# Optimization experiments

Measured on AMD Instinct MI355X. Metric: run time of the kernel, lower is better.

## Reference

```python
import jax, jax.numpy as jnp
import numpy as np

B, CIN, COUT, N, R = 8, 64, 64, 32768, 32
R3 = R * R * R
BN_EPS = 1e-4


def leaky(x):
    return jnp.where(x >= 0, x, 0.1 * x)


def bn(x, gamma, beta, axes, bshape):
    # training-mode batchnorm (batch statistics)
    m = x.mean(axes, keepdims=True)
    v = x.var(axes, keepdims=True)
    return (x - m) * jax.lax.rsqrt(v + BN_EPS) * gamma.reshape(bshape) + beta.reshape(bshape)


def conv3d(x, w, b):
    y = jax.lax.conv_general_dilated(
        x, w, window_strides=(1, 1, 1), padding=[(1, 1)] * 3,
        dimension_numbers=('NCDHW', 'OIDHW', 'NCDHW'))
    return y + b[None, :, None, None, None]


def setup_inputs() -> dict:
    key = jax.random.key(0)
    ks = jax.random.split(key, 6)
    f32 = jnp.float32
    return {
        'features': jax.random.normal(ks[0], (B, CIN, N), f32),
        'coords': jax.random.normal(ks[1], (B, 3, N), f32),
        'w1': jax.random.normal(ks[2], (COUT, CIN, 3, 3, 3), f32) * 0.05,
        'b1': jnp.zeros((COUT,), f32),
        'g1': jnp.ones((COUT,), f32),
        'beta1': jnp.zeros((COUT,), f32),
        'w2': jax.random.normal(ks[3], (COUT, COUT, 3, 3, 3), f32) * 0.05,
        'b2': jnp.zeros((COUT,), f32),
        'g2': jnp.ones((COUT,), f32),
        'beta2': jnp.zeros((COUT,), f32),
        'wp': jax.random.normal(ks[4], (COUT, CIN), f32) * 0.05,
        'bp': jnp.zeros((COUT,), f32),
        'gp': jnp.ones((COUT,), f32),
        'betap': jnp.zeros((COUT,), f32),
    }


def _norm_coords(coords):
    # Voxelization coordinate normalization (normalize=True, eps=0)
    nc = coords - coords.mean(axis=2, keepdims=True)                      # [B,3,N]
    mag = jnp.linalg.norm(nc, axis=1, keepdims=True)                      # [B,1,N]
    nc = nc / (mag.max(axis=2, keepdims=True) * 2.0) + 0.5
    return jnp.clip(nc * R, 0.0, R - 1)                                   # [B,3,N] in [0, R-1]


def _voxelize(features, norm):
    vox = jnp.round(norm).astype(jnp.int32)                               # [B,3,N]
    flat = (vox[:, 0] * R + vox[:, 1]) * R + vox[:, 2]                    # [B,N]

    def scat(f, idx):  # f: [C,N], idx: [N]
        s = jax.ops.segment_sum(f.T, idx, num_segments=R3)                # [R3,C]
        c = jax.ops.segment_sum(jnp.ones(idx.shape, f.dtype), idx, num_segments=R3)
        return (s / jnp.maximum(c, 1.0)[:, None]).T                       # [C,R3]

    return jax.vmap(scat)(features, flat)                                 # [B,C,R3]


def _devoxelize(grid_flat, norm):
    # trilinear gather: grid_flat [B,C,R3], norm [B,3,N] -> [B,C,N]
    lo = jnp.floor(norm).astype(jnp.int32)
    frac = norm - lo
    hi = jnp.clip(lo + 1, 0, R - 1)
    gather = jax.vmap(lambda gf, i: gf[:, i])  # per-batch fancy gather
    out = jnp.zeros((grid_flat.shape[0], grid_flat.shape[1], norm.shape[2]), grid_flat.dtype)
    for dx in (0, 1):
        for dy in (0, 1):
            for dz in (0, 1):
                xi = hi[:, 0] if dx else lo[:, 0]
                yi = hi[:, 1] if dy else lo[:, 1]
                zi = hi[:, 2] if dz else lo[:, 2]
                w = ((frac[:, 0] if dx else 1.0 - frac[:, 0]) *
                     (frac[:, 1] if dy else 1.0 - frac[:, 1]) *
                     (frac[:, 2] if dz else 1.0 - frac[:, 2]))            # [B,N]
                idx = (xi * R + yi) * R + zi                               # [B,N]
                out = out + gather(grid_flat, idx) * w[:, None, :]
    return out


def reference(features, coords, w1, b1, g1, beta1, w2, b2, g2, beta2, wp, bp, gp, betap):
    norm = _norm_coords(coords)
    grid = _voxelize(features, norm).reshape(B, CIN, R, R, R)
    x = leaky(bn(conv3d(grid, w1, b1), g1, beta1, (0, 2, 3, 4), (1, COUT, 1, 1, 1)))
    x = leaky(bn(conv3d(x, w2, b2), g2, beta2, (0, 2, 3, 4), (1, COUT, 1, 1, 1)))
    voxel_feats = _devoxelize(x.reshape(B, COUT, R3), norm)               # [B,COUT,N]
    # point branch: SharedMLP = 1x1 Conv1d + BN1d + ReLU
    p = jnp.einsum('oc,bcn->bon', wp, features) + bp[None, :, None]
    p = jax.nn.relu(bn(p, gp, betap, (0, 2), (1, COUT, 1)))
    return voxel_feats + p
```

## Files before the change

kernel.cpp:

```cpp
#include <hip/hip_runtime.h>

typedef __attribute__((ext_vector_type(8))) short short8;
typedef __attribute__((ext_vector_type(8))) unsigned short ushort8;
typedef __attribute__((ext_vector_type(4))) unsigned short ushort4v;
typedef __attribute__((ext_vector_type(4))) float f32x4;
typedef unsigned int uint;
typedef unsigned short ushort;

#define BB 8
#define CC 64
#define NPT 32768
#define RR 32
#define R3 32768
#define RP 34
#define RP2 1156
#define RP3 39304
#define BN_EPS 1e-4f

__device__ __forceinline__ ushort f2bf(float x) {
    uint u = __float_as_uint(x);
    u = (u + 0x7FFFu + ((u >> 16) & 1u)) >> 16;
    return (ushort)u;
}
__device__ __forceinline__ float bf2f(ushort u) {
    return __uint_as_float(((uint)u) << 16);
}
__device__ __forceinline__ void gload_lds16(const void* g, void* l) {
    __builtin_amdgcn_global_load_lds(
        (const __attribute__((address_space(1))) unsigned int*)g,
        (__attribute__((address_space(3))) unsigned int*)l, 16, 0, 0);
}

__global__ void k_mean(const float* __restrict__ coords, float* __restrict__ mean) {
    __shared__ float sbuf[256];
    int bd = blockIdx.x;
    const float* c = coords + (size_t)bd * NPT;
    float s = 0.f;
    for (int i = threadIdx.x; i < NPT; i += 256) s += c[i];
    sbuf[threadIdx.x] = s; __syncthreads();
    for (int off = 128; off > 0; off >>= 1) {
        if (threadIdx.x < off) sbuf[threadIdx.x] += sbuf[threadIdx.x + off];
        __syncthreads();
    }
    if (threadIdx.x == 0) mean[bd] = sbuf[0] / (float)NPT;
}

__global__ void k_maxmag(const float* __restrict__ coords, const float* __restrict__ mean,
                         float* __restrict__ maxmag) {
    __shared__ float sbuf[256];
    int b = blockIdx.x;
    float m0 = mean[b*3], m1 = mean[b*3+1], m2 = mean[b*3+2];
    const float* c = coords + (size_t)b * 3 * NPT;
    float mx = 0.f;
    for (int i = threadIdx.x; i < NPT; i += 256) {
        float x = c[i] - m0, y = c[NPT + i] - m1, z = c[2*NPT + i] - m2;
        mx = fmaxf(mx, x*x + y*y + z*z);
    }
    sbuf[threadIdx.x] = mx; __syncthreads();
    for (int off = 128; off > 0; off >>= 1) {
        if (threadIdx.x < off) sbuf[threadIdx.x] = fmaxf(sbuf[threadIdx.x], sbuf[threadIdx.x + off]);
        __syncthreads();
    }
    if (threadIdx.x == 0) maxmag[b] = sqrtf(sbuf[0]);
}

__global__ void k_norm(const float* __restrict__ coords, const float* __restrict__ mean,
                       const float* __restrict__ maxmag,
                       float* __restrict__ norm, int* __restrict__ nxt, int* __restrict__ head) {
    int b = blockIdx.y;
    int n = blockIdx.x * 256 + threadIdx.x;
    float denom = maxmag[b] * 2.0f;
    int vi[3];
    #pragma unroll
    for (int d = 0; d < 3; d++) {
        float v = (coords[((size_t)b*3 + d)*NPT + n] - mean[b*3 + d]) / denom + 0.5f;
        v *= (float)RR;
        v = fminf(fmaxf(v, 0.0f), (float)(RR - 1));
        norm[((size_t)b*3 + d)*NPT + n] = v;
        vi[d] = (int)rintf(v);
    }
    int pf = ((vi[0]+1)*RP + (vi[1]+1))*RP + (vi[2]+1);
    nxt[b*NPT + n] = atomicExch(&head[b*RP3 + pf], n);
}

__global__ __launch_bounds__(256) void k_transpose(const float* __restrict__ feat,
                                                   ushort* __restrict__ featT) {
    __shared__ float t[64][65];
    int b = blockIdx.y;
    int n0 = blockIdx.x * 64;
    for (int i = threadIdx.x; i < 4096; i += 256) {
        int ci = i >> 6, nl = i & 63;
        t[ci][nl] = feat[((size_t)(b*CC + ci))*NPT + n0 + nl];
    }
    __syncthreads();
    for (int i = threadIdx.x; i < 4096; i += 256) {
        int nl = i >> 6, ci = i & 63;
        featT[((size_t)b*NPT + n0 + nl)*64 + ci] = f2bf(t[ci][nl]);
    }
}

__global__ __launch_bounds__(256) void k_gather(const ushort* __restrict__ featT,
                                                const int* __restrict__ head,
                                                const int* __restrict__ nxt,
                                                ushort* __restrict__ gbf) {
    int b = blockIdx.y;
    int v = blockIdx.x * 4 + (threadIdx.x >> 6);
    int lane = threadIdx.x & 63;
    float a = 0.f;
    int c = 0;
    int p = head[b*RP3 + v];
    while (p >= 0) {
        a += bf2f(featT[((size_t)b*NPT + p)*64 + lane]);
        c++;
        p = nxt[b*NPT + p];
    }
    float r = (c > 0) ? a / (float)c : 0.f;
    gbf[((size_t)((b*2 + (lane >> 5))*RP3) + v)*32 + (lane & 31)] = f2bf(r);
}

__global__ void k_wt(const float* __restrict__ w, ushort* __restrict__ wT) {
    int s = blockIdx.x * 256 + threadIdx.x;
    int ci = s & 31;
    int co = (s >> 5) & 63;
    int t  = (s >> 11) % 27;
    int ch = s / 55296;
    wT[s] = f2bf(w[(size_t)co*1728 + (size_t)(ch*32 + ci)*27 + t]);
}

__global__ void k_bnpack(const ushort* __restrict__ raw,
                         const float* __restrict__ gs, const float* __restrict__ gq,
                         const float* __restrict__ gamma, const float* __restrict__ beta,
                         ushort* __restrict__ gbf) {
    __shared__ float s_sc[64], s_sh[64];
    if (threadIdx.x < 64) {
        int c = threadIdx.x;
        const float cntf = 262144.0f;
        float m = gs[c] / cntf;
        float vv = gq[c] / cntf - m*m;
        float scv = gamma[c] * rsqrtf(fmaxf(vv, 0.0f) + BN_EPS);
        s_sc[c] = scv;
        s_sh[c] = beta[c] - m*scv;
    }
    __syncthreads();
    int s = blockIdx.x * 256 + threadIdx.x;
    int j = s & 3;
    int tmp = s >> 2;
    int v = tmp % RP3;
    int t2 = tmp / RP3;
    int ch = t2 & 1, b = t2 >> 1;
    int gz = v / RP2; int r = v - gz*RP2;
    int gy = r / RP;  int gx = r - gy*RP;
    ushort8 o;
    if (gz >= 1 && gz <= 32 && gy >= 1 && gy <= 32 && gx >= 1 && gx <= 32) {
        int uvox = ((gz-1)*RR + (gy-1))*RR + (gx-1);
        int cb = ch*32 + j*8;
        ushort8 rv = *(const ushort8*)(raw + ((size_t)b*R3 + uvox)*64 + cb);
        #pragma unroll
        for (int e = 0; e < 8; e++) {
            float x = bf2f(rv[e])*s_sc[cb + e] + s_sh[cb + e];
            x = x >= 0.f ? x : 0.1f*x;
            o[e] = f2bf(x);
        }
    } else {
        #pragma unroll
        for (int e = 0; e < 8; e++) o[e] = 0;
    }
    *(ushort8*)(gbf + ((size_t)((b*2 + ch)*RP3) + v)*32 + j*8) = o;
}

__global__ __launch_bounds__(512) void k_conv_mfma(
    const ushort* __restrict__ gbf,
    const ushort* __restrict__ wT,
    ushort* __restrict__ rawbf,
    float* __restrict__ gs, float* __restrict__ gq)
{
    __shared__ uint4 lds4[2 * 3888];
    const int d0r = blockIdx.x;
    const int d0 = (d0r & 7) * 4 + (d0r >> 3);
    const int quad = blockIdx.y, b = blockIdx.z;
    const int y0 = (quad >> 1) * 16, x0 = (quad & 1) * 16;
    const int tid = threadIdx.x;
    const int lane = tid & 63;
    const int wid = tid >> 6;
    const int mgroup = wid & 1, ngroup = wid >> 1;
    const int l15 = lane & 15, kgrp = lane >> 4;

    f32x4 acc[2][4];
    #pragma unroll
    for (int mf = 0; mf < 2; mf++)
        #pragma unroll
        for (int f = 0; f < 4; f++) acc[mf][f] = (f32x4)(0.0f);

    const int coA = mgroup*32 + l15;
    const int coB = coA + 16;

    {
        const char* gbase = (const char*)gbf + (size_t)(b*2 + 0) * ((size_t)RP3 * 64);
        for (int c = tid; c < 3888; c += 512) {
            int row = c >> 2, j = c & 3;
            int z = row / 324; int rem = row - z*324;
            int y = rem / 18;  int xl = rem - y*18;
            int srcj = j ^ ((xl >> 1) & 3);
            const char* src = gbase +
                (size_t)((d0 + z)*RP2 + (y0 + y)*RP + (x0 + xl)) * 64 + srcj*16;
            gload_lds16(src, (char*)lds4 + c*16);
        }
    }
    __syncthreads();
    {
        const char* gbase = (const char*)gbf + (size_t)(b*2 + 1) * ((size_t)RP3 * 64);
        for (int c = tid; c < 3888; c += 512) {
            int row = c >> 2, j = c & 3;
            int z = row / 324; int rem = row - z*324;
            int y = rem / 18;  int xl = rem - y*18;
            int srcj = j ^ ((xl >> 1) & 3);
            const char* src = gbase +
                (size_t)((d0 + z)*RP2 + (y0 + y)*RP + (x0 + xl)) * 64 + srcj*16;
            gload_lds16(src, (char*)lds4 + 62208 + c*16);
        }
    }

    #pragma unroll
    for (int ch = 0; ch < 2; ch++) {
        if (ch == 1) __syncthreads();
        const char* lbase = (const char*)lds4 + ch * 62208;
        const ushort* wbase = wT + (size_t)ch * 27 * 2048 + kgrp*8;
        short8 wq[3][2];
        #pragma unroll
        for (int pre = 0; pre < 3; pre++) {
            wq[pre][0] = *(const short8*)(wbase + (size_t)pre*2048 + coA*32);
            wq[pre][1] = *(const short8*)(wbase + (size_t)pre*2048 + coB*32);
        }
        __builtin_amdgcn_s_setprio(1);
        #pragma unroll
        for (int t = 0; t < 27; t++) {
            const int t0 = t / 9, t1 = (t / 3) % 3, t2 = t % 3;
            const int slot = t % 3;
            int x = l15 + t2;
            int inrow = (kgrp ^ ((x >> 1) & 3)) << 4;
            #pragma unroll
            for (int f = 0; f < 4; f++) {
                int y = ngroup*4 + f + t1;
                int vox = (t0*18 + y)*18 + x;
                short8 bfr = *(const short8*)(lbase + vox*64 + inrow);
                acc[0][f] = __builtin_amdgcn_mfma_f32_16x16x32_bf16(wq[slot][0], bfr, acc[0][f], 0, 0, 0);
                acc[1][f] = __builtin_amdgcn_mfma_f32_16x16x32_bf16(wq[slot][1], bfr, acc[1][f], 0, 0, 0);
            }
            if (t + 3 < 27) {
                wq[slot][0] = *(const short8*)(wbase + (size_t)(t+3)*2048 + coA*32);
                wq[slot][1] = *(const short8*)(wbase + (size_t)(t+3)*2048 + coB*32);
            }
        }
        __builtin_amdgcn_s_setprio(0);
    }
    int d2 = x0 + l15;
    #pragma unroll
    for (int f = 0; f < 4; f++) {
        int d1 = y0 + ngroup*4 + f;
        int vox = (d0*RR + d1)*RR + d2;
        ushort* dst = rawbf + ((size_t)b*R3 + vox)*64 + mgroup*32 + kgrp*4;
        ushort4v o0, o1;
        #pragma unroll
        for (int e = 0; e < 4; e++) { o0[e] = f2bf(acc[0][f][e]); o1[e] = f2bf(acc[1][f][e]); }
        *(ushort4v*)dst = o0;
        *(ushort4v*)(dst + 16) = o1;
    }
    __syncthreads();
    float* bins = (float*)lds4;
    if (tid < 128) bins[tid] = 0.f;
    __syncthreads();
    float sv[2][4], qv[2][4];
    #pragma unroll
    for (int mf = 0; mf < 2; mf++)
        #pragma unroll
        for (int e = 0; e < 4; e++) {
            float s = 0.f, q = 0.f;
            #pragma unroll
            for (int f = 0; f < 4; f++) {
                float v = acc[mf][f][e];
                s += v; q += v*v;
            }
            #pragma unroll
            for (int m = 1; m < 16; m <<= 1) {
                s += __shfl_xor(s, m);
                q += __shfl_xor(q, m);
            }
            sv[mf][e] = s; qv[mf][e] = q;
        }
    if (l15 == 0) {
        #pragma unroll
        for (int mf = 0; mf < 2; mf++)
            #pragma unroll
            for (int e = 0; e < 4; e++) {
                int co = mgroup*32 + mf*16 + kgrp*4 + e;
                atomicAdd(&bins[co], sv[mf][e]);
                atomicAdd(&bins[64 + co], qv[mf][e]);
            }
    }
    __syncthreads();
    if (tid < 64) { atomicAdd(&gs[tid], bins[tid]); atomicAdd(&gq[tid], bins[64 + tid]); }
}

__global__ __launch_bounds__(256) void k_point_stats_P(const ushort* __restrict__ featT,
                                                       const float* __restrict__ wp,
                                                       ushort* __restrict__ P,
                                                       float* __restrict__ gs,
                                                       float* __restrict__ gq) {
    __shared__ float ls[64], lq[64];
    int b = blockIdx.y;
    int n = blockIdx.x * 256 + threadIdx.x;
    if (threadIdx.x < 64) { ls[threadIdx.x] = 0.f; lq[threadIdx.x] = 0.f; }
    __syncthreads();
    f32x4 fr[16];
    const ushort8* fp = (const ushort8*)(featT + ((size_t)b*NPT + n)*64);
    #pragma unroll
    for (int r = 0; r < 8; r++) {
        ushort8 u = fp[r];
        #pragma unroll
        for (int e = 0; e < 8; e++)
            fr[(r*8 + e) >> 2][(r*8 + e) & 3] = bf2f(u[e]);
    }
    int lane = threadIdx.x & 63;
    #pragma unroll
    for (int co = 0; co < 64; co++) {
        float p = 0.f;
        #pragma unroll
        for (int r = 0; r < 16; r++) {
            f32x4 w4 = *(const f32x4*)(wp + co*64 + r*4);
            p = fmaf(w4[0], fr[r][0], p); p = fmaf(w4[1], fr[r][1], p);
            p = fmaf(w4[2], fr[r][2], p); p = fmaf(w4[3], fr[r][3], p);
        }
        P[((size_t)(b*64 + co))*NPT + n] = f2bf(p);
        float s = p, q = p*p;
        #pragma unroll
        for (int m = 1; m < 64; m <<= 1) {
            s += __shfl_xor(s, m);
            q += __shfl_xor(q, m);
        }
        if (lane == 0) { atomicAdd(&ls[co], s); atomicAdd(&lq[co], q); }
    }
    __syncthreads();
    if (threadIdx.x < 64) {
        atomicAdd(&gs[threadIdx.x], ls[threadIdx.x]);
        atomicAdd(&gq[threadIdx.x], lq[threadIdx.x]);
    }
}

__global__ __launch_bounds__(256) void k_final4(
    const ushort* __restrict__ x2raw,
    const float* __restrict__ norm,
    const ushort* __restrict__ P,
    const float* __restrict__ gs2, const float* __restrict__ gq2,
    const float* __restrict__ g2, const float* __restrict__ be2,
    const float* __restrict__ gsp, const float* __restrict__ gqp,
    const float* __restrict__ gp, const float* __restrict__ bep,
    float* __restrict__ out)
{
    __shared__ float s_sc[64], s_sh[64], s_scp[64], s_shp[64];
    int b = blockIdx.y;
    int tid = threadIdx.x;
    const float cntf = 262144.0f;
    if (tid < 64) {
        int c = tid;
        float m = gs2[c] / cntf;
        float vv = gq2[c] / cntf - m*m;
        float scv = g2[c] * rsqrtf(fmaxf(vv, 0.0f) + BN_EPS);
        s_sc[c] = scv; s_sh[c] = be2[c] - m*scv;
    } else if (tid < 128) {
        int c = tid - 64;
        float m = gsp[c] / cntf;
        float vv = gqp[c] / cntf - m*m;
        float scv = gp[c] * rsqrtf(fmaxf(vv, 0.0f) + BN_EPS);
        s_scp[c] = scv; s_shp[c] = bep[c] - m*scv;
    }
    __syncthreads();
    int pt = blockIdx.x * 64 + (tid & 63);
    int q = tid >> 6;
    float v0 = norm[((size_t)b*3 + 0)*NPT + pt];
    float v1 = norm[((size_t)b*3 + 1)*NPT + pt];
    float v2 = norm[((size_t)b*3 + 2)*NPT + pt];
    int l0 = (int)floorf(v0), l1 = (int)floorf(v1), l2 = (int)floorf(v2);
    float f0 = v0 - (float)l0, f1 = v1 - (float)l1, f2 = v2 - (float)l2;
    int h0 = min(l0 + 1, RR - 1), h1 = min(l1 + 1, RR - 1), h2 = min(l2 + 1, RR - 1);

    f32x4 scv[4], shv[4];
    #pragma unroll
    for (int r = 0; r < 4; r++) {
        scv[r] = *(const f32x4*)&s_sc[q*16 + r*4];
        shv[r] = *(const f32x4*)&s_sh[q*16 + r*4];
    }

    f32x4 a4[4];
    #pragma unroll
    for (int r = 0; r < 4; r++) a4[r] = (f32x4)(0.0f);
    #pragma unroll
    for (int c = 0; c < 8; c++) {
        int xi = (c & 4) ? h0 : l0; float wx = (c & 4) ? f0 : 1.f - f0;
        int yi = (c & 2) ? h1 : l1; float wy = (c & 2) ? f1 : 1.f - f1;
        int zi = (c & 1) ? h2 : l2; float wz = (c & 1) ? f2 : 1.f - f2;
        float w = wx * wy * wz;
        const ushort* g = x2raw +
            ((size_t)b*R3 + (size_t)((xi*RR + yi)*RR + zi))*64 + q*16;
        ushort8 rv0 = *(const ushort8*)g;
        ushort8 rv1 = *(const ushort8*)(g + 8);
        #pragma unroll
        for (int r = 0; r < 2; r++) {
            #pragma unroll
            for (int e = 0; e < 4; e++) {
                float x = bf2f(rv0[r*4 + e])*scv[r][e] + shv[r][e];
                x = x >= 0.f ? x : 0.1f*x;
                a4[r][e] = fmaf(w, x, a4[r][e]);
                float x2 = bf2f(rv1[r*4 + e])*scv[2 + r][e] + shv[2 + r][e];
                x2 = x2 >= 0.f ? x2 : 0.1f*x2;
                a4[2 + r][e] = fmaf(w, x2, a4[2 + r][e]);
            }
        }
    }
    #pragma unroll
    for (int r = 0; r < 4; r++) {
        #pragma unroll
        for (int e = 0; e < 4; e++) {
            int co = q*16 + r*4 + e;
            float p = bf2f(P[((size_t)(b*64 + co))*NPT + pt]);
            p = p * s_scp[co] + s_shp[co];
            p = fmaxf(p, 0.f);
            out[((size_t)(b*64 + co))*NPT + pt] = a4[r][e] + p;
        }
    }
}

extern "C" void kernel_launch(void* const* d_in, const int* in_sizes, int n_in,
                              void* d_out, int out_size, void* d_ws, size_t ws_size,
                              hipStream_t stream) {
    const float* feat   = (const float*)d_in[0];
    const float* coords = (const float*)d_in[1];
    const float* w1  = (const float*)d_in[2];
    const float* g1  = (const float*)d_in[4];
    const float* be1 = (const float*)d_in[5];
    const float* w2  = (const float*)d_in[6];
    const float* g2  = (const float*)d_in[8];
    const float* be2 = (const float*)d_in[9];
    const float* wp  = (const float*)d_in[10];
    const float* gp  = (const float*)d_in[12];
    const float* bep = (const float*)d_in[13];
    float* out = (float*)d_out;
    float* ws  = (float*)d_ws;

    float* mean   = ws;
    float* maxmag = ws + 24;
    float* stats  = ws + 32;
    float* norm   = ws + 1024;
    int*   nxt    = (int*)(ws + 787456);
    int*   head   = (int*)(ws + 1049600);
    ushort* rawbf = (ushort*)(ws + 1364032);
    ushort* wT1   = (ushort*)(ws + 21487680);
    ushort* wT2   = (ushort*)(ws + 21542976);
    ushort* gbf   = (ushort*)(ws + 21598272);
    ushort* P     = (ushort*)(ws + 21598272);
    ushort* featT = (ushort*)(ws + 31660096);

    hipMemsetAsync(stats, 0, 384 * sizeof(float), stream);
    hipMemsetAsync(head, 0xFF, 314432ull * sizeof(int), stream);

    k_wt<<<432, 256, 0, stream>>>(w1, wT1);
    k_wt<<<432, 256, 0, stream>>>(w2, wT2);

    k_mean  <<<24, 256, 0, stream>>>(coords, mean);
    k_maxmag<<<8, 256, 0, stream>>>(coords, mean, maxmag);
    k_norm  <<<dim3(128, 8), 256, 0, stream>>>(coords, mean, maxmag, norm, nxt, head);
    k_transpose<<<dim3(512, 8), 256, 0, stream>>>(feat, featT);
    k_gather<<<dim3(9826, 8), 256, 0, stream>>>(featT, head, nxt, gbf);

    k_conv_mfma<<<dim3(32, 4, 8), 512, 0, stream>>>(gbf, wT1, rawbf, stats + 0, stats + 64);
    k_bnpack<<<9826, 256, 0, stream>>>(rawbf, stats + 0, stats + 64, g1, be1, gbf);

    k_conv_mfma<<<dim3(32, 4, 8), 512, 0, stream>>>(gbf, wT2, rawbf, stats + 128, stats + 192);

    k_point_stats_P<<<dim3(128, 8), 256, 0, stream>>>(featT, wp, P, stats + 256, stats + 320);

    k_final4<<<dim3(512, 8), 256, 0, stream>>>(rawbf, norm, P,
                                               stats + 128, stats + 192, g2, be2,
                                               stats + 256, stats + 320, gp, bep,
                                               out);
}
```

Before: 494.8 us.

## Fuse coord prep kernels, merge weight transposes, store point-MLP output point-major

Merges the mean, max-magnitude and normalize/link-list kernels into one per-batch 1024-thread kernel, and folds the two weight-transpose launches into one. The point MLP now writes its bf16 output in place over featT, in point-major layout with vector stores, and the final kernel reads it with two 16-byte loads instead of 16 strided scalar loads. This cuts launch count and makes the P write and read coalesced. The cost is that normalization now runs on only 8 blocks, which serializes a pass over the coordinates that was previously spread across 1024 blocks.

Result: slower. 557.2 us (+12.6%).

```diff
diff --git a/kernel.cpp b/kernel.cpp
--- a/kernel.cpp
+++ b/kernel.cpp
@@ -31,56 +31,53 @@
         (__attribute__((address_space(3))) unsigned int*)l, 16, 0, 0);
 }
 
-__global__ void k_mean(const float* __restrict__ coords, float* __restrict__ mean) {
-    __shared__ float sbuf[256];
-    int bd = blockIdx.x;
-    const float* c = coords + (size_t)bd * NPT;
-    float s = 0.f;
-    for (int i = threadIdx.x; i < NPT; i += 256) s += c[i];
-    sbuf[threadIdx.x] = s; __syncthreads();
-    for (int off = 128; off > 0; off >>= 1) {
-        if (threadIdx.x < off) sbuf[threadIdx.x] += sbuf[threadIdx.x + off];
+__global__ __launch_bounds__(1024) void k_prep(const float* __restrict__ coords,
+                                               float* __restrict__ norm,
+                                               int* __restrict__ nxt, int* __restrict__ head) {
+    __shared__ float sb[1024];
+    __shared__ float sm[4];
+    int b = blockIdx.x;
+    int tid = threadIdx.x;
+    const float* cb = coords + (size_t)b * 3 * NPT;
+    #pragma unroll
+    for (int d = 0; d < 3; d++) {
+        float s = 0.f;
+        for (int i = tid; i < NPT; i += 1024) s += cb[(size_t)d*NPT + i];
+        sb[tid] = s; __syncthreads();
+        for (int off = 512; off > 0; off >>= 1) {
+            if (tid < off) sb[tid] += sb[tid + off];
+            __syncthreads();
+        }
+        if (tid == 0) sm[d] = sb[0] / (float)NPT;
         __syncthreads();
     }
-    if (threadIdx.x == 0) mean[bd] = sbuf[0] / (float)NPT;
-}
-
-__global__ void k_maxmag(const float* __restrict__ coords, const float* __restrict__ mean,
-                         float* __restrict__ maxmag) {
-    __shared__ float sbuf[256];
-    int b = blockIdx.x;
-    float m0 = mean[b*3], m1 = mean[b*3+1], m2 = mean[b*3+2];
-    const float* c = coords + (size_t)b * 3 * NPT;
+    float m0 = sm[0], m1 = sm[1], m2 = sm[2];
     float mx = 0.f;
-    for (int i = threadIdx.x; i < NPT; i += 256) {
-        float x = c[i] - m0, y = c[NPT + i] - m1, z = c[2*NPT + i] - m2;
+    for (int i = tid; i < NPT; i += 1024) {
+        float x = cb[i] - m0, y = cb[NPT + i] - m1, z = cb[2*NPT + i] - m2;
         mx = fmaxf(mx, x*x + y*y + z*z);
     }
-    sbuf[threadIdx.x] = mx; __syncthreads();
-    for (int off = 128; off > 0; off >>= 1) {
-        if (threadIdx.x < off) sbuf[threadIdx.x] = fmaxf(sbuf[threadIdx.x], sbuf[threadIdx.x + off]);
+    sb[tid] = mx; __syncthreads();
+    for (int off = 512; off > 0; off >>= 1) {
+        if (tid < off) sb[tid] = fmaxf(sb[tid], sb[tid + off]);
         __syncthreads();
     }
-    if (threadIdx.x == 0) maxmag[b] = sqrtf(sbuf[0]);
-}
-
-__global__ void k_norm(const float* __restrict__ coords, const float* __restrict__ mean,
-                       const float* __restrict__ maxmag,
-                       float* __restrict__ norm, int* __restrict__ nxt, int* __restrict__ head) {
-    int b = blockIdx.y;
-    int n = blockIdx.x * 256 + threadIdx.x;
-    float denom = maxmag[b] * 2.0f;
-    int vi[3];
-    #pragma unroll
-    for (int d = 0; d < 3; d++) {
-        float v = (coords[((size_t)b*3 + d)*NPT + n] - mean[b*3 + d]) / denom + 0.5f;
-        v *= (float)RR;
-        v = fminf(fmaxf(v, 0.0f), (float)(RR - 1));
-        norm[((size_t)b*3 + d)*NPT + n] = v;
-        vi[d] = (int)rintf(v);
-    }
-    int pf = ((vi[0]+1)*RP + (vi[1]+1))*RP + (vi[2]+1);
-    nxt[b*NPT + n] = atomicExch(&head[b*RP3 + pf], n);
+    if (tid == 0) sm[3] = sqrtf(sb[0]) * 2.0f;
+    __syncthreads();
+    float denom = sm[3];
+    for (int n = tid; n < NPT; n += 1024) {
+        float v0 = (cb[n] - m0) / denom + 0.5f;
+        float v1 = (cb[NPT + n] - m1) / denom + 0.5f;
+        float v2 = (cb[2*NPT + n] - m2) / denom + 0.5f;
+        v0 = fminf(fmaxf(v0 * (float)RR, 0.f), (float)(RR - 1));
+        v1 = fminf(fmaxf(v1 * (float)RR, 0.f), (float)(RR - 1));
+        v2 = fminf(fmaxf(v2 * (float)RR, 0.f), (float)(RR - 1));
+        norm[((size_t)b*3 + 0)*NPT + n] = v0;
+        norm[((size_t)b*3 + 1)*NPT + n] = v1;
+        norm[((size_t)b*3 + 2)*NPT + n] = v2;
+        int pf = (((int)rintf(v0)+1)*RP + ((int)rintf(v1)+1))*RP + ((int)rintf(v2)+1);
+        nxt[b*NPT + n] = atomicExch(&head[b*RP3 + pf], n);
+    }
 }
 
 __global__ __launch_bounds__(256) void k_transpose(const float* __restrict__ feat,
@@ -118,13 +115,17 @@
     gbf[((size_t)((b*2 + (lane >> 5))*RP3) + v)*32 + (lane & 31)] = f2bf(r);
 }
 
-__global__ void k_wt(const float* __restrict__ w, ushort* __restrict__ wT) {
+__global__ void k_wt2(const float* __restrict__ w1, const float* __restrict__ w2,
+                      ushort* __restrict__ wT1, ushort* __restrict__ wT2) {
     int s = blockIdx.x * 256 + threadIdx.x;
-    int ci = s & 31;
-    int co = (s >> 5) & 63;
-    int t  = (s >> 11) % 27;
-    int ch = s / 55296;
-    wT[s] = f2bf(w[(size_t)co*1728 + (size_t)(ch*32 + ci)*27 + t]);
+    const float* w = (s < 110592) ? w1 : w2;
+    ushort* wT = (s < 110592) ? wT1 : wT2;
+    int si = (s < 110592) ? s : s - 110592;
+    int ci = si & 31;
+    int co = (si >> 5) & 63;
+    int t  = (si >> 11) % 27;
+    int ch = si / 55296;
+    wT[si] = f2bf(w[(size_t)co*1728 + (size_t)(ch*32 + ci)*27 + t]);
 }
 
 __global__ void k_bnpack(const ushort* __restrict__ raw,
@@ -301,9 +302,8 @@
     if (tid < 64) { atomicAdd(&gs[tid], bins[tid]); atomicAdd(&gq[tid], bins[64 + tid]); }
 }
 
-__global__ __launch_bounds__(256) void k_point_stats_P(const ushort* __restrict__ featT,
+__global__ __launch_bounds__(256) void k_point_stats_P(ushort* __restrict__ featT,
                                                        const float* __restrict__ wp,
-                                                       ushort* __restrict__ P,
                                                        float* __restrict__ gs,
                                                        float* __restrict__ gq) {
     __shared__ float ls[64], lq[64];
@@ -311,26 +311,29 @@
     int n = blockIdx.x * 256 + threadIdx.x;
     if (threadIdx.x < 64) { ls[threadIdx.x] = 0.f; lq[threadIdx.x] = 0.f; }
     __syncthreads();
-    f32x4 fr[16];
-    const ushort8* fp = (const ushort8*)(featT + ((size_t)b*NPT + n)*64);
-    #pragma unroll
-    for (int r = 0; r < 8; r++) {
-        ushort8 u = fp[r];
-        #pragma unroll
-        for (int e = 0; e < 8; e++)
-            fr[(r*8 + e) >> 2][(r*8 + e) & 3] = bf2f(u[e]);
+    ushort* rowp = featT + ((size_t)b*NPT + n)*64;
+    float fr[64];
+    {
+        const ushort8* fp = (const ushort8*)rowp;
+        #pragma unroll
+        for (int r = 0; r < 8; r++) {
+            ushort8 u = fp[r];
+            #pragma unroll
+            for (int e = 0; e < 8; e++) fr[r*8 + e] = bf2f(u[e]);
+        }
     }
     int lane = threadIdx.x & 63;
+    float ps[64];
     #pragma unroll
     for (int co = 0; co < 64; co++) {
         float p = 0.f;
         #pragma unroll
         for (int r = 0; r < 16; r++) {
             f32x4 w4 = *(const f32x4*)(wp + co*64 + r*4);
-            p = fmaf(w4[0], fr[r][0], p); p = fmaf(w4[1], fr[r][1], p);
-            p = fmaf(w4[2], fr[r][2], p); p = fmaf(w4[3], fr[r][3], p);
-        }
-        P[((size_t)(b*64 + co))*NPT + n] = f2bf(p);
+            p = fmaf(w4[0], fr[r*4+0], p); p = fmaf(w4[1], fr[r*4+1], p);
+            p = fmaf(w4[2], fr[r*4+2], p); p = fmaf(w4[3], fr[r*4+3], p);
+        }
+        ps[co] = p;
         float s = p, q = p*p;
         #pragma unroll
         for (int m = 1; m < 64; m <<= 1) {
@@ -338,6 +341,13 @@
             q += __shfl_xor(q, m);
         }
         if (lane == 0) { atomicAdd(&ls[co], s); atomicAdd(&lq[co], q); }
+    }
+    #pragma unroll
+    for (int g = 0; g < 8; g++) {
+        ushort8 o;
+        #pragma unroll
+        for (int e = 0; e < 8; e++) o[e] = f2bf(ps[g*8 + e]);
+        *(ushort8*)(rowp + g*8) = o;
     }
     __syncthreads();
     if (threadIdx.x < 64) {
@@ -416,12 +426,16 @@
             }
         }
     }
+    const ushort* pr = P + ((size_t)b*NPT + pt)*64 + q*16;
+    ushort8 pv0 = *(const ushort8*)pr;
+    ushort8 pv1 = *(const ushort8*)(pr + 8);
     #pragma unroll
     for (int r = 0; r < 4; r++) {
         #pragma unroll
         for (int e = 0; e < 4; e++) {
-            int co = q*16 + r*4 + e;
-            float p = bf2f(P[((size_t)(b*64 + co))*NPT + pt]);
+            int idx = r*4 + e;
+            int co = q*16 + idx;
+            float p = bf2f(idx < 8 ? pv0[idx] : pv1[idx - 8]);
             p = p * s_scp[co] + s_shp[co];
             p = fmaxf(p, 0.f);
             out[((size_t)(b*64 + co))*NPT + pt] = a4[r][e] + p;
@@ -446,8 +460,7 @@
     float* out = (float*)d_out;
     float* ws  = (float*)d_ws;
 
-    float* mean   = ws;
-    float* maxmag = ws + 24;
+    float* mean_unused = ws;  (void)mean_unused;
     float* stats  = ws + 32;
     float* norm   = ws + 1024;
     int*   nxt    = (int*)(ws + 787456);
@@ -456,18 +469,13 @@
     ushort* wT1   = (ushort*)(ws + 21487680);
     ushort* wT2   = (ushort*)(ws + 21542976);
     ushort* gbf   = (ushort*)(ws + 21598272);
-    ushort* P     = (ushort*)(ws + 21598272);
     ushort* featT = (ushort*)(ws + 31660096);
 
     hipMemsetAsync(stats, 0, 384 * sizeof(float), stream);
     hipMemsetAsync(head, 0xFF, 314432ull * sizeof(int), stream);
 
-    k_wt<<<432, 256, 0, stream>>>(w1, wT1);
-    k_wt<<<432, 256, 0, stream>>>(w2, wT2);
-
-    k_mean  <<<24, 256, 0, stream>>>(coords, mean);
-    k_maxmag<<<8, 256, 0, stream>>>(coords, mean, maxmag);
-    k_norm  <<<dim3(128, 8), 256, 0, stream>>>(coords, mean, maxmag, norm, nxt, head);
+    k_wt2<<<864, 256, 0, stream>>>(w1, w2, wT1, wT2);
+    k_prep<<<8, 1024, 0, stream>>>(coords, norm, nxt, head);
     k_transpose<<<dim3(512, 8), 256, 0, stream>>>(feat, featT);
     k_gather<<<dim3(9826, 8), 256, 0, stream>>>(featT, head, nxt, gbf);
 
@@ -476,9 +484,9 @@
 
     k_conv_mfma<<<dim3(32, 4, 8), 512, 0, stream>>>(gbf, wT2, rawbf, stats + 128, stats + 192);
 
-    k_point_stats_P<<<dim3(128, 8), 256, 0, stream>>>(featT, wp, P, stats + 256, stats + 320);
-
-    k_final4<<<dim3(512, 8), 256, 0, stream>>>(rawbf, norm, P,
+    k_point_stats_P<<<dim3(128, 8), 256, 0, stream>>>(featT, wp, stats + 256, stats + 320);
+
+    k_final4<<<dim3(512, 8), 256, 0, stream>>>(rawbf, norm, featT,
                                                stats + 128, stats + 192, g2, be2,
                                                stats + 256, stats + 320, gp, bep,
                                                out);
```
